# Kernel optimization log

Measured on AMD Instinct MI355X. Metric: run time of the kernel, lower is better.

The kernel has to match this reference:

```python
import jax, jax.numpy as jnp
import numpy as np

K = 2  # number of propagation hops (init arg k)


def setup_inputs() -> dict:
    key = jax.random.key(0)
    k1, k2, k3 = jax.random.split(key, 3)
    N, E, D = 100000, 1200000, 64
    feat = jax.random.normal(k1, (N, D), dtype=jnp.float32)
    src = jax.random.randint(k2, (E,), 0, N, dtype=jnp.int32)
    dst = jax.random.randint(k3, (E,), 0, N, dtype=jnp.int32)
    return {"feat": feat, "src": src, "dst": dst, "n_nodes": N}


def reference(feat, src, dst, n_nodes):
    # in-degree normalization: norm = clamp(in_deg, 1)^-0.5, shape [N, 1]
    deg = jax.ops.segment_sum(
        jnp.ones(dst.shape, dtype=feat.dtype), dst, num_segments=n_nodes
    )
    norm = jnp.power(jnp.maximum(deg, 1.0), -0.5)[:, None]
    for _ in range(K):
        feat = feat * norm                      # pre-scale by D^-1/2
        msgs = feat[src]                        # copy_u: gather source features [E, D]
        feat = jax.ops.segment_sum(msgs, dst, num_segments=n_nodes)  # sum at dst
        feat = feat * norm                      # post-scale by D^-1/2
    return feat
```

## Files before the change

kernel.cpp:

```cpp
#include <hip/hip_runtime.h>
#include <hip/hip_fp16.h>

#define D 64
#define BSH2 8
#define NPB 256
#define NB2_MAX 512
#define PCHUNK 4096
#define CAPP 6144
#define CAP2 4096

typedef float f32x4 __attribute__((ext_vector_type(4)));


__global__ void zero_f32(float* __restrict__ p, long n) {
    long i = (long)blockIdx.x * blockDim.x + threadIdx.x;
    long stride = (long)gridDim.x * blockDim.x;
    for (; i < n; i += stride) p[i] = 0.0f;
}

__global__ void init_cursors(int* __restrict__ gcur, int NB2) {
    int i = blockIdx.x * blockDim.x + threadIdx.x;
    if (i < NB2) gcur[i << 4] = i * CAPP;
}

__global__ __launch_bounds__(1024) void partition_direct(const int* __restrict__ src,
                                                         const int* __restrict__ dst,
                                                         int* __restrict__ gcur,
                                                         int* __restrict__ packed,
                                                         int E, int NB2) {
    __shared__ int staged[PCHUNK];
    __shared__ int lhist[NB2_MAX];
    __shared__ int lbase[NB2_MAX];
    __shared__ int lcur[NB2_MAX];
    __shared__ int gbase[NB2_MAX];
    int tid = threadIdx.x;
    int c0 = blockIdx.x * PCHUNK;
    int c1 = c0 + PCHUNK; if (c1 > E) c1 = E;

    if (tid < NB2_MAX) lhist[tid] = 0;
    __syncthreads();

    for (int e = c0 + tid * 4; e + 4 <= c1; e += 4096) {
        int4 d4 = *(const int4*)(dst + e);
        atomicAdd(&lhist[d4.x >> BSH2], 1);
        atomicAdd(&lhist[d4.y >> BSH2], 1);
        atomicAdd(&lhist[d4.z >> BSH2], 1);
        atomicAdd(&lhist[d4.w >> BSH2], 1);
    }
    int tail = c0 + ((c1 - c0) & ~3);
    for (int e = tail + tid; e < c1; e += 1024)
        atomicAdd(&lhist[dst[e] >> BSH2], 1);
    __syncthreads();

    if (tid < 64) {
        const int CPL = NB2_MAX / 64;
        int tmp[CPL];
        int s = 0;
        int base = tid * CPL;
        #pragma unroll
        for (int j = 0; j < CPL; j++) { tmp[j] = s; s += lhist[base + j]; }
        int incl = s;
        #pragma unroll
        for (int o = 1; o < 64; o <<= 1) {
            int t = __shfl_up(incl, o, 64);
            if (tid >= o) incl += t;
        }
        int excl = incl - s;
        #pragma unroll
        for (int j = 0; j < CPL; j++) {
            lbase[base + j] = excl + tmp[j];
            lcur[base + j]  = excl + tmp[j];
        }
    }
    __syncthreads();

    for (int e = c0 + tid * 4; e + 4 <= c1; e += 4096) {
        int4 d4 = *(const int4*)(dst + e);
        int4 s4 = *(const int4*)(src + e);
        int k, pos;
        k = d4.x >> BSH2; pos = atomicAdd(&lcur[k], 1);
        staged[pos] = s4.x | ((d4.x & (NPB - 1)) << 20);
        k = d4.y >> BSH2; pos = atomicAdd(&lcur[k], 1);
        staged[pos] = s4.y | ((d4.y & (NPB - 1)) << 20);
        k = d4.z >> BSH2; pos = atomicAdd(&lcur[k], 1);
        staged[pos] = s4.z | ((d4.z & (NPB - 1)) << 20);
        k = d4.w >> BSH2; pos = atomicAdd(&lcur[k], 1);
        staged[pos] = s4.w | ((d4.w & (NPB - 1)) << 20);
    }
    for (int e = tail + tid; e < c1; e += 1024) {
        int d = dst[e];
        int k = d >> BSH2;
        int pos = atomicAdd(&lcur[k], 1);
        staged[pos] = src[e] | ((d & (NPB - 1)) << 20);
    }
    __syncthreads();

    if (tid < NB2_MAX && tid < NB2) {
        int c = lhist[tid];
        gbase[tid] = c ? atomicAdd(&gcur[tid << 4], (c + 15) & ~15) : 0;
    }
    __syncthreads();

    int grp = tid >> 4, sub = tid & 15;
    for (int k = grp; k < NB2; k += 64) {
        int c = lhist[k];
        if (!c) continue;
        int c16 = (c + 15) & ~15;
        int g = gbase[k], base = lbase[k];
        for (int i = sub; i < c16; i += 16)
            packed[g + i] = (i < c) ? staged[base + i] : -1;
    }
}

__global__ __launch_bounds__(1024) void bucket_csr(const int* __restrict__ packed,
                                                   const int* __restrict__ gcur,
                                                   int2* __restrict__ rbc,
                                                   float* __restrict__ norm,
                                                   float* __restrict__ norm2,
                                                   int* __restrict__ csr,
                                                   const float4* __restrict__ feat,
                                                   uint2* __restrict__ fq,
                                                   int N, int NB2) {
    __shared__ int cnt[NPB];
    __shared__ int loc[NPB];
    int b = blockIdx.x;
    int tid = threadIdx.x;
    if (tid < NPB) cnt[tid] = 0;
    __syncthreads();

    int rbeg = b * CAPP;
    int rend = gcur[b << 4];
    for (int e = rbeg + tid * 4; e + 4 <= rend; e += 4096) {
        int4 p4 = *(const int4*)(packed + e);
        if (p4.x != -1) atomicAdd(&cnt[(p4.x >> 20) & (NPB - 1)], 1);
        if (p4.y != -1) atomicAdd(&cnt[(p4.y >> 20) & (NPB - 1)], 1);
        if (p4.z != -1) atomicAdd(&cnt[(p4.z >> 20) & (NPB - 1)], 1);
        if (p4.w != -1) atomicAdd(&cnt[(p4.w >> 20) & (NPB - 1)], 1);
    }
    __syncthreads();
    if (tid < 64) {
        int tmp[4];
        int s = 0;
        int base = tid * 4;
        #pragma unroll
        for (int j = 0; j < 4; j++) { tmp[j] = s; s += cnt[base + j]; }
        int incl = s;
        #pragma unroll
        for (int o = 1; o < 64; o <<= 1) {
            int t = __shfl_up(incl, o, 64);
            if (tid >= o) incl += t;
        }
        int excl = incl - s;
        #pragma unroll
        for (int j = 0; j < 4; j++) loc[base + j] = excl + tmp[j];
    }
    __syncthreads();

    int cbase = b * CAP2;
    if (tid < NPB) {
        int node = (b << BSH2) + tid;
        if (node < N) {
            int v = cnt[tid];
            int ep = loc[tid];
            rbc[node] = make_int2(cbase + ep, v);
            float df = (float)v; df = df < 1.0f ? 1.0f : df;
            float r = rsqrtf(df);
            norm[node] = r;
            norm2[node] = r * r;
        }
    }
    __syncthreads();
    for (int e = rbeg + tid * 4; e + 4 <= rend; e += 4096) {
        int4 p4 = *(const int4*)(packed + e);
        int l, pos;
        if (p4.x != -1) { l = (p4.x >> 20) & (NPB - 1); pos = atomicAdd(&loc[l], 1); csr[cbase + pos] = p4.x & 0xFFFFF; }
        if (p4.y != -1) { l = (p4.y >> 20) & (NPB - 1); pos = atomicAdd(&loc[l], 1); csr[cbase + pos] = p4.y & 0xFFFFF; }
        if (p4.z != -1) { l = (p4.z >> 20) & (NPB - 1); pos = atomicAdd(&loc[l], 1); csr[cbase + pos] = p4.z & 0xFFFFF; }
        if (p4.w != -1) { l = (p4.w >> 20) & (NPB - 1); pos = atomicAdd(&loc[l], 1); csr[cbase + pos] = p4.w & 0xFFFFF; }
    }

    #pragma unroll
    for (int it = 0; it < 4; it++) {
        int item = tid + it * 1024;
        int l = item >> 4;
        int node = (b << BSH2) + l;
        if (node < N) {
            int t = item & 15;
            float4 v = feat[(long)node * 16 + t];
            float df = (float)cnt[l]; df = df < 1.0f ? 1.0f : df;
            float r = rsqrtf(df);
            __half2 a = __floats2half2_rn(v.x * r, v.y * r);
            __half2 bb = __floats2half2_rn(v.z * r, v.w * r);
            uint2 u;
            u.x = *(unsigned int*)&a;
            u.y = *(unsigned int*)&bb;
            fq[(long)node * 16 + t] = u;
        }
    }
}

template <int NS>
__device__ __forceinline__ void burst(const uint4* __restrict__ x16,
                                      const int* __restrict__ csr,
                                      int beg, int deg, int off,
                                      int g, int sub, float* a) {
    int e[NS]; float m[NS]; int s[NS]; uint4 u[NS];
    #pragma unroll
    for (int i = 0; i < NS; i++) {
        int idx = g + off + 8 * i;
        bool v = idx < deg;
        e[i] = v ? beg + idx : beg;
        m[i] = v ? 1.f : 0.f;
    }
    #pragma unroll
    for (int i = 0; i < NS; i++) s[i] = csr[e[i]];
    #pragma unroll
    for (int i = 0; i < NS; i++) u[i] = x16[s[i] * 8 + sub];
    #pragma unroll
    for (int i = 0; i < NS; i++) {
        float2 f;
        f = __half22float2(*(const __half2*)&u[i].x); a[0] += f.x * m[i]; a[1] += f.y * m[i];
        f = __half22float2(*(const __half2*)&u[i].y); a[2] += f.x * m[i]; a[3] += f.y * m[i];
        f = __half22float2(*(const __half2*)&u[i].z); a[4] += f.x * m[i]; a[5] += f.y * m[i];
        f = __half22float2(*(const __half2*)&u[i].w); a[6] += f.x * m[i]; a[7] += f.y * m[i];
    }
}

template <bool OUTHALF>
__global__ __launch_bounds__(256) void gather_row(const __half* __restrict__ x,
                                                  const int2* __restrict__ rbc,
                                                  const int* __restrict__ csr,
                                                  const float* __restrict__ post,
                                                  void* __restrict__ outv, int N) {
    int w = blockIdx.x * 4 + (threadIdx.x >> 6);
    if (w >= N) return;
    int lane = threadIdx.x & 63;
    int g = lane >> 3;
    int sub = lane & 7;
    int2 bc = rbc[w];
    int beg = bc.x, deg = bc.y;
    const uint4* x16 = (const uint4*)x;
    float pn = post[w];
    float a[8];
    #pragma unroll
    for (int i = 0; i < 8; i++) a[i] = 0.f;

    if (deg > 0) {
        if (deg <= 8) {
            burst<1>(x16, csr, beg, deg, 0, g, sub, a);
        } else if (deg <= 16) {
            burst<2>(x16, csr, beg, deg, 0, g, sub, a);
        } else if (deg <= 32) {
            burst<4>(x16, csr, beg, deg, 0, g, sub, a);
        } else {
            for (int off = 0; off < deg; off += 32)
                burst<4>(x16, csr, beg, deg, off, g, sub, a);
        }
    }

    #pragma unroll
    for (int i = 0; i < 8; i++) {
        a[i] += __shfl_xor(a[i], 8, 64);
        a[i] += __shfl_xor(a[i], 16, 64);
        a[i] += __shfl_xor(a[i], 32, 64);
    }
    if (g == 0) {
        #pragma unroll
        for (int i = 0; i < 8; i++) a[i] *= pn;
        if (OUTHALF) {
            __half2 h0 = __floats2half2_rn(a[0], a[1]);
            __half2 h1 = __floats2half2_rn(a[2], a[3]);
            __half2 h2 = __floats2half2_rn(a[4], a[5]);
            __half2 h3 = __floats2half2_rn(a[6], a[7]);
            uint4 u;
            u.x = *(unsigned int*)&h0;
            u.y = *(unsigned int*)&h1;
            u.z = *(unsigned int*)&h2;
            u.w = *(unsigned int*)&h3;
            ((uint4*)outv)[(long)w * 8 + sub] = u;
        } else {
            f32x4 r0; r0.x = a[0]; r0.y = a[1]; r0.z = a[2]; r0.w = a[3];
            f32x4 r1; r1.x = a[4]; r1.y = a[5]; r1.z = a[6]; r1.w = a[7];
            __builtin_nontemporal_store(r0, ((f32x4*)outv) + (long)w * 16 + sub * 2);
            __builtin_nontemporal_store(r1, ((f32x4*)outv) + (long)w * 16 + sub * 2 + 1);
        }
    }
}


__global__ void deg_kernel_f(const int* __restrict__ dst, float* __restrict__ deg, int E) {
    int e = blockIdx.x * blockDim.x + threadIdx.x;
    if (e < E) unsafeAtomicAdd(&deg[dst[e]], 1.0f);
}

__global__ void norm_kernel_f(float* __restrict__ deg_norm, float* __restrict__ norm2, int N) {
    int i = blockIdx.x * blockDim.x + threadIdx.x;
    if (i < N) {
        float d = deg_norm[i];
        d = d < 1.0f ? 1.0f : d;
        float r = rsqrtf(d);
        deg_norm[i] = r;
        norm2[i] = r * r;
    }
}

__global__ void scatter_kernel(const float* __restrict__ x,
                               const float* __restrict__ scale,
                               const int* __restrict__ src,
                               const int* __restrict__ dst,
                               float* __restrict__ out, int E) {
    long idx = (long)blockIdx.x * blockDim.x + threadIdx.x;
    int e = (int)(idx >> 6);
    int lane = (int)(idx & 63);
    if (e < E) {
        int s = src[e];
        int d0 = dst[e];
        float v = x[(long)s * D + lane] * scale[s];
        unsafeAtomicAdd(&out[(long)d0 * D + lane], v);
    }
}

__global__ void scale_kernel(float* __restrict__ out, const float* __restrict__ norm, long n) {
    long i = (long)blockIdx.x * blockDim.x + threadIdx.x;
    if (i < n) out[i] *= norm[i >> 6];
}


extern "C" void kernel_launch(void* const* d_in, const int* in_sizes, int n_in,
                              void* d_out, int out_size, void* d_ws, size_t ws_size,
                              hipStream_t stream) {
    const float* feat = (const float*)d_in[0];
    const int*   src  = (const int*)d_in[1];
    const int*   dst  = (const int*)d_in[2];
    float* out = (float*)d_out;

    const int N = in_sizes[0] / D;
    const int E = in_sizes[1];
    const long ND = (long)N * D;
    const int NB2 = (N + NPB - 1) >> BSH2;

    long o_gcur = 0;
    long o_rbc  = o_gcur + NB2_MAX * 16;
    long o_norm = o_rbc + 2L * N;
    long o_norm2 = o_norm + N;
    long o_csr  = (o_norm2 + N + 3) & ~3L;
    long o_f16  = (o_csr + (long)NB2 * CAP2 + 3) & ~3L;
    long o_buf1 = (o_f16 + ND / 2 + 3) & ~3L;
    long pk_len = (long)NB2 * CAPP;
    long buf1_len = (ND / 2 > pk_len) ? ND / 2 : pk_len;
    size_t need = (size_t)(o_buf1 + buf1_len) * 4;

    if (ws_size >= need && N <= (1 << 20) && NB2 <= NB2_MAX) {
        int*   bi = (int*)d_ws;
        float* bf = (float*)d_ws;
        int* gcur    = bi + o_gcur;
        int2* rbc    = (int2*)(bi + o_rbc);
        float* norm  = bf + o_norm;
        float* norm2 = bf + o_norm2;
        int* csr     = bi + o_csr;
        __half* feat16 = (__half*)(bi + o_f16);
        __half* buf1h  = (__half*)(bi + o_buf1);
        int* packed  = bi + o_buf1;

        int pblocks = (E + PCHUNK - 1) / PCHUNK;

        init_cursors<<<(NB2 + 255) / 256, 256, 0, stream>>>(gcur, NB2);
        partition_direct<<<pblocks, 1024, 0, stream>>>(src, dst, gcur, packed, E, NB2);
        bucket_csr<<<NB2, 1024, 0, stream>>>(packed, gcur, rbc, norm, norm2, csr,
                                             (const float4*)feat, (uint2*)feat16, N, NB2);

        int gblocks = (N + 3) / 4;
        gather_row<true><<<gblocks, 256, 0, stream>>>(feat16, rbc, csr, norm2, buf1h, N);
        gather_row<false><<<gblocks, 256, 0, stream>>>(buf1h, rbc, csr, norm, out, N);
    } else {
        float* norm  = (float*)d_ws;
        float* norm2 = norm + N;
        float* buf1  = norm2 + N;

        long nz = 2L * N + ND;
        zero_f32<<<(int)((nz + 255) / 256), 256, 0, stream>>>((float*)d_ws, nz);
        zero_f32<<<(int)((ND + 255) / 256), 256, 0, stream>>>(out, ND);
        deg_kernel_f<<<(E + 255) / 256, 256, 0, stream>>>(dst, norm, E);
        norm_kernel_f<<<(N + 255) / 256, 256, 0, stream>>>(norm, norm2, N);
        long work = (long)E * D;
        int blocks = (int)((work + 255) / 256);
        scatter_kernel<<<blocks, 256, 0, stream>>>(feat, norm, src, dst, buf1, E);
        scatter_kernel<<<blocks, 256, 0, stream>>>(buf1, norm2, src, dst, out, E);
        scale_kernel<<<(int)((ND + 255) / 256), 256, 0, stream>>>(out, norm, ND);
    }
}
```

Measured before the change: 171.0 us.

## Build CSR with global atomic degree histogram and direct placement

Replaces the two-pass shared-memory bucket partition (partition_direct plus bucket_csr) with a simpler counting sort. It zeroes the degrees, builds a per-node degree histogram with global atomics, computes per-node offsets and norms, then places each edge's source through per-node global atomic cursors. This drops the packed intermediate buffer and its extra read/write passes. In exchange it relies on scattered, value-returning global atomics, and the neighbour order within each row becomes nondeterministic.

```diff
diff --git a/kernel.cpp b/kernel.cpp
--- a/kernel.cpp
+++ b/kernel.cpp
@@ -5,8 +5,6 @@
 #define BSH2 8
 #define NPB 256
 #define NB2_MAX 512
-#define PCHUNK 4096
-#define CAPP 6144
 #define CAP2 4096
 
 typedef float f32x4 __attribute__((ext_vector_type(4)));
@@ -18,126 +16,40 @@
     for (; i < n; i += stride) p[i] = 0.0f;
 }
 
-__global__ void init_cursors(int* __restrict__ gcur, int NB2) {
+__global__ __launch_bounds__(256) void deg_hist(const int* __restrict__ dst,
+                                                int* __restrict__ deg, int E) {
     int i = blockIdx.x * blockDim.x + threadIdx.x;
-    if (i < NB2) gcur[i << 4] = i * CAPP;
-}
-
-__global__ __launch_bounds__(1024) void partition_direct(const int* __restrict__ src,
-                                                         const int* __restrict__ dst,
-                                                         int* __restrict__ gcur,
-                                                         int* __restrict__ packed,
-                                                         int E, int NB2) {
-    __shared__ int staged[PCHUNK];
-    __shared__ int lhist[NB2_MAX];
-    __shared__ int lbase[NB2_MAX];
-    __shared__ int lcur[NB2_MAX];
-    __shared__ int gbase[NB2_MAX];
-    int tid = threadIdx.x;
-    int c0 = blockIdx.x * PCHUNK;
-    int c1 = c0 + PCHUNK; if (c1 > E) c1 = E;
-
-    if (tid < NB2_MAX) lhist[tid] = 0;
-    __syncthreads();
-
-    for (int e = c0 + tid * 4; e + 4 <= c1; e += 4096) {
+    int e = i * 4;
+    if (e + 4 <= E) {
         int4 d4 = *(const int4*)(dst + e);
-        atomicAdd(&lhist[d4.x >> BSH2], 1);
-        atomicAdd(&lhist[d4.y >> BSH2], 1);
-        atomicAdd(&lhist[d4.z >> BSH2], 1);
-        atomicAdd(&lhist[d4.w >> BSH2], 1);
-    }
-    int tail = c0 + ((c1 - c0) & ~3);
-    for (int e = tail + tid; e < c1; e += 1024)
-        atomicAdd(&lhist[dst[e] >> BSH2], 1);
-    __syncthreads();
-
-    if (tid < 64) {
-        const int CPL = NB2_MAX / 64;
-        int tmp[CPL];
-        int s = 0;
-        int base = tid * CPL;
-        #pragma unroll
-        for (int j = 0; j < CPL; j++) { tmp[j] = s; s += lhist[base + j]; }
-        int incl = s;
-        #pragma unroll
-        for (int o = 1; o < 64; o <<= 1) {
-            int t = __shfl_up(incl, o, 64);
-            if (tid >= o) incl += t;
-        }
-        int excl = incl - s;
-        #pragma unroll
-        for (int j = 0; j < CPL; j++) {
-            lbase[base + j] = excl + tmp[j];
-            lcur[base + j]  = excl + tmp[j];
-        }
-    }
-    __syncthreads();
-
-    for (int e = c0 + tid * 4; e + 4 <= c1; e += 4096) {
-        int4 d4 = *(const int4*)(dst + e);
-        int4 s4 = *(const int4*)(src + e);
-        int k, pos;
-        k = d4.x >> BSH2; pos = atomicAdd(&lcur[k], 1);
-        staged[pos] = s4.x | ((d4.x & (NPB - 1)) << 20);
-        k = d4.y >> BSH2; pos = atomicAdd(&lcur[k], 1);
-        staged[pos] = s4.y | ((d4.y & (NPB - 1)) << 20);
-        k = d4.z >> BSH2; pos = atomicAdd(&lcur[k], 1);
-        staged[pos] = s4.z | ((d4.z & (NPB - 1)) << 20);
-        k = d4.w >> BSH2; pos = atomicAdd(&lcur[k], 1);
-        staged[pos] = s4.w | ((d4.w & (NPB - 1)) << 20);
-    }
-    for (int e = tail + tid; e < c1; e += 1024) {
-        int d = dst[e];
-        int k = d >> BSH2;
-        int pos = atomicAdd(&lcur[k], 1);
-        staged[pos] = src[e] | ((d & (NPB - 1)) << 20);
-    }
-    __syncthreads();
-
-    if (tid < NB2_MAX && tid < NB2) {
-        int c = lhist[tid];
-        gbase[tid] = c ? atomicAdd(&gcur[tid << 4], (c + 15) & ~15) : 0;
-    }
-    __syncthreads();
-
-    int grp = tid >> 4, sub = tid & 15;
-    for (int k = grp; k < NB2; k += 64) {
-        int c = lhist[k];
-        if (!c) continue;
-        int c16 = (c + 15) & ~15;
-        int g = gbase[k], base = lbase[k];
-        for (int i = sub; i < c16; i += 16)
-            packed[g + i] = (i < c) ? staged[base + i] : -1;
-    }
-}
-
-__global__ __launch_bounds__(1024) void bucket_csr(const int* __restrict__ packed,
-                                                   const int* __restrict__ gcur,
-                                                   int2* __restrict__ rbc,
-                                                   float* __restrict__ norm,
-                                                   float* __restrict__ norm2,
-                                                   int* __restrict__ csr,
-                                                   const float4* __restrict__ feat,
-                                                   uint2* __restrict__ fq,
-                                                   int N, int NB2) {
+        atomicAdd(&deg[d4.x], 1);
+        atomicAdd(&deg[d4.y], 1);
+        atomicAdd(&deg[d4.z], 1);
+        atomicAdd(&deg[d4.w], 1);
+    } else {
+        for (; e < E; e++) atomicAdd(&deg[dst[e]], 1);
+    }
+}
+
+__global__ __launch_bounds__(1024) void node_init(const int* __restrict__ deg,
+                                                  int2* __restrict__ rbc,
+                                                  int* __restrict__ cursor,
+                                                  float* __restrict__ norm,
+                                                  float* __restrict__ norm2,
+                                                  const float4* __restrict__ feat,
+                                                  uint2* __restrict__ fq,
+                                                  int N) {
     __shared__ int cnt[NPB];
     __shared__ int loc[NPB];
     int b = blockIdx.x;
     int tid = threadIdx.x;
-    if (tid < NPB) cnt[tid] = 0;
+
+    if (tid < NPB) {
+        int node = (b << BSH2) + tid;
+        cnt[tid] = (node < N) ? deg[node] : 0;
+    }
     __syncthreads();
 
-    int rbeg = b * CAPP;
-    int rend = gcur[b << 4];
-    for (int e = rbeg + tid * 4; e + 4 <= rend; e += 4096) {
-        int4 p4 = *(const int4*)(packed + e);
-        if (p4.x != -1) atomicAdd(&cnt[(p4.x >> 20) & (NPB - 1)], 1);
-        if (p4.y != -1) atomicAdd(&cnt[(p4.y >> 20) & (NPB - 1)], 1);
-        if (p4.z != -1) atomicAdd(&cnt[(p4.z >> 20) & (NPB - 1)], 1);
-        if (p4.w != -1) atomicAdd(&cnt[(p4.w >> 20) & (NPB - 1)], 1);
-    }
-    __syncthreads();
     if (tid < 64) {
         int tmp[4];
         int s = 0;
@@ -161,22 +73,14 @@
         int node = (b << BSH2) + tid;
         if (node < N) {
             int v = cnt[tid];
-            int ep = loc[tid];
-            rbc[node] = make_int2(cbase + ep, v);
+            int beg = cbase + loc[tid];
+            rbc[node] = make_int2(beg, v);
+            cursor[node] = beg;
             float df = (float)v; df = df < 1.0f ? 1.0f : df;
             float r = rsqrtf(df);
             norm[node] = r;
             norm2[node] = r * r;
         }
-    }
-    __syncthreads();
-    for (int e = rbeg + tid * 4; e + 4 <= rend; e += 4096) {
-        int4 p4 = *(const int4*)(packed + e);
-        int l, pos;
-        if (p4.x != -1) { l = (p4.x >> 20) & (NPB - 1); pos = atomicAdd(&loc[l], 1); csr[cbase + pos] = p4.x & 0xFFFFF; }
-        if (p4.y != -1) { l = (p4.y >> 20) & (NPB - 1); pos = atomicAdd(&loc[l], 1); csr[cbase + pos] = p4.y & 0xFFFFF; }
-        if (p4.z != -1) { l = (p4.z >> 20) & (NPB - 1); pos = atomicAdd(&loc[l], 1); csr[cbase + pos] = p4.z & 0xFFFFF; }
-        if (p4.w != -1) { l = (p4.w >> 20) & (NPB - 1); pos = atomicAdd(&loc[l], 1); csr[cbase + pos] = p4.w & 0xFFFFF; }
     }
 
     #pragma unroll
@@ -195,6 +99,28 @@
             u.x = *(unsigned int*)&a;
             u.y = *(unsigned int*)&bb;
             fq[(long)node * 16 + t] = u;
+        }
+    }
+}
+
+__global__ __launch_bounds__(256) void place(const int* __restrict__ src,
+                                             const int* __restrict__ dst,
+                                             int* __restrict__ cursor,
+                                             int* __restrict__ csr, int E) {
+    int i = blockIdx.x * blockDim.x + threadIdx.x;
+    int e = i * 4;
+    if (e + 4 <= E) {
+        int4 d4 = *(const int4*)(dst + e);
+        int4 s4 = *(const int4*)(src + e);
+        int p;
+        p = atomicAdd(&cursor[d4.x], 1); csr[p] = s4.x;
+        p = atomicAdd(&cursor[d4.y], 1); csr[p] = s4.y;
+        p = atomicAdd(&cursor[d4.z], 1); csr[p] = s4.z;
+        p = atomicAdd(&cursor[d4.w], 1); csr[p] = s4.w;
+    } else {
+        for (; e < E; e++) {
+            int p = atomicAdd(&cursor[dst[e]], 1);
+            csr[p] = src[e];
         }
     }
 }
@@ -339,35 +265,34 @@
     const long ND = (long)N * D;
     const int NB2 = (N + NPB - 1) >> BSH2;
 
-    long o_gcur = 0;
-    long o_rbc  = o_gcur + NB2_MAX * 16;
-    long o_norm = o_rbc + 2L * N;
+    long o_rbc   = 0;
+    long o_norm  = o_rbc + 2L * N;
     long o_norm2 = o_norm + N;
-    long o_csr  = (o_norm2 + N + 3) & ~3L;
-    long o_f16  = (o_csr + (long)NB2 * CAP2 + 3) & ~3L;
-    long o_buf1 = (o_f16 + ND / 2 + 3) & ~3L;
-    long pk_len = (long)NB2 * CAPP;
-    long buf1_len = (ND / 2 > pk_len) ? ND / 2 : pk_len;
-    size_t need = (size_t)(o_buf1 + buf1_len) * 4;
-
-    if (ws_size >= need && N <= (1 << 20) && NB2 <= NB2_MAX) {
+    long o_deg   = o_norm2 + N;
+    long o_cur   = o_deg + N;
+    long o_csr   = (o_cur + N + 3) & ~3L;
+    long o_f16   = o_csr + (long)NB2 * CAP2;
+    long o_b1    = o_f16 + ND / 2;
+    size_t need = (size_t)(o_b1 + ND / 2) * 4;
+
+    if (ws_size >= need && N <= NB2_MAX * NPB) {
         int*   bi = (int*)d_ws;
         float* bf = (float*)d_ws;
-        int* gcur    = bi + o_gcur;
         int2* rbc    = (int2*)(bi + o_rbc);
         float* norm  = bf + o_norm;
         float* norm2 = bf + o_norm2;
+        int* deg     = bi + o_deg;
+        int* cursor  = bi + o_cur;
         int* csr     = bi + o_csr;
         __half* feat16 = (__half*)(bi + o_f16);
-        __half* buf1h  = (__half*)(bi + o_buf1);
-        int* packed  = bi + o_buf1;
-
-        int pblocks = (E + PCHUNK - 1) / PCHUNK;
-
-        init_cursors<<<(NB2 + 255) / 256, 256, 0, stream>>>(gcur, NB2);
-        partition_direct<<<pblocks, 1024, 0, stream>>>(src, dst, gcur, packed, E, NB2);
-        bucket_csr<<<NB2, 1024, 0, stream>>>(packed, gcur, rbc, norm, norm2, csr,
-                                             (const float4*)feat, (uint2*)feat16, N, NB2);
+        __half* buf1h  = (__half*)(bi + o_b1);
+
+        zero_f32<<<(N + 255) / 256, 256, 0, stream>>>((float*)deg, N);
+        int hblocks = (E / 4 + 255) / 256 + 1;
+        deg_hist<<<hblocks, 256, 0, stream>>>(dst, deg, E);
+        node_init<<<NB2, 1024, 0, stream>>>(deg, rbc, cursor, norm, norm2,
+                                            (const float4*)feat, (uint2*)feat16, N);
+        place<<<hblocks, 256, 0, stream>>>(src, dst, cursor, csr, E);
 
         int gblocks = (N + 3) / 4;
         gather_row<true><<<gblocks, 256, 0, stream>>>(feat16, rbc, csr, norm2, buf1h, N);
```

Measured after the change: 274.7 us. 1.61x slower.
